# Performance work log

Measured on AMD Instinct MI355X. Metric: run time of the kernel, lower is better.

The kernel has to match this reference:

```python
import jax, jax.numpy as jnp
import numpy as np

B, T, D_MODEL, HEAD_DIM = 8, 2048, 1024, 128


def setup_inputs() -> dict:
    key = jax.random.key(0)
    k1, k2, k3, k4 = jax.random.split(key, 4)
    scale = 1.0 / np.sqrt(D_MODEL)
    return {
        "x": jax.random.normal(k1, (B, T, D_MODEL), dtype=jnp.float32),
        "Wq": jax.random.normal(k2, (HEAD_DIM, D_MODEL), dtype=jnp.float32) * scale,
        "Wk": jax.random.normal(k3, (HEAD_DIM, D_MODEL), dtype=jnp.float32) * scale,
        "Wv": jax.random.normal(k4, (HEAD_DIM, D_MODEL), dtype=jnp.float32) * scale,
    }


def reference(x, Wq, Wk, Wv) -> jnp.ndarray:
    # x: [B, T, C]; torch Linear(no bias): y = x @ W.T, W: [head_dim, d_model]
    q = jnp.einsum("btc,hc->bth", x, Wq)  # [B, T, H]
    k = jnp.einsum("btc,hc->bth", x, Wk)
    v = jnp.einsum("btc,hc->bth", x, Wv)
    head_dim = Wq.shape[0]
    scores = jnp.einsum("bqh,bkh->bqk", q, k) / jnp.sqrt(jnp.float32(head_dim))  # [B, T, T]
    T_ = x.shape[1]
    causal = jnp.tril(jnp.ones((T_, T_), dtype=bool))
    scores = jnp.where(causal, scores, -jnp.inf)
    probs = jax.nn.softmax(scores, axis=-1)
    # dropout is identity at inference (eval mode)
    out = jnp.einsum("bqk,bkh->bqh", probs, v)  # [B, T, head_dim]
    return out
```

## Files before the change

kernel.cpp:

```cpp
#include <hip/hip_runtime.h>
#include <hip/hip_bf16.h>
#include <math.h>

#define T_ 2048
#define C_ 1024
#define H_ 128
#define NB 8
#define WN 131072
#define SC 0.08838834764831845f

typedef __attribute__((ext_vector_type(8))) short bf16x8;
typedef __attribute__((ext_vector_type(8))) unsigned short u16x8;
typedef __attribute__((ext_vector_type(4))) float f32x4;

#define MFMA16(a,b,c) __builtin_amdgcn_mfma_f32_16x16x32_bf16((a),(b),(c),0,0,0)

__device__ __forceinline__ unsigned short f2bf(float f) {
    union { float f; unsigned u; } v; v.f = f;
    unsigned r = v.u + 0x7fffu + ((v.u >> 16) & 1u);
    return (unsigned short)(r >> 16);
}
__device__ __forceinline__ float bf2f(unsigned short u) {
    union { unsigned u; float f; } v; v.u = ((unsigned)u) << 16; return v.f;
}
__device__ __forceinline__ unsigned pk2bf(float a, float b) {
    __hip_bfloat162 h = __float22bfloat162_rn(float2{a, b});
    union { __hip_bfloat162 h; unsigned u; } v; v.h = h; return v.u;
}
__device__ __forceinline__ void gld16(void* lds, const void* g) {
    __builtin_amdgcn_global_load_lds(
        (const __attribute__((address_space(1))) unsigned*)g,
        (__attribute__((address_space(3))) unsigned*)lds, 16, 0, 0);
}

__global__ __launch_bounds__(256) void wconv(const float* __restrict__ Wq,
                                             const float* __restrict__ Wk,
                                             const float* __restrict__ Wv,
                                             unsigned short* __restrict__ Wb) {
    int e = (blockIdx.x * 256 + threadIdx.x) * 8;
    int which = e >> 17;
    int off = e & (WN - 1);
    const float* src = (which == 0) ? Wq : (which == 1 ? Wk : Wv);
    float s = (which == 0) ? SC : 1.0f;
    const float4* p = (const float4*)(src + off);
    float4 a = p[0], b = p[1];
    uint4 o = { pk2bf(a.x * s, a.y * s), pk2bf(a.z * s, a.w * s),
                pk2bf(b.x * s, b.y * s), pk2bf(b.z * s, b.w * s) };
    *(uint4*)(Wb + e) = o;
}

__global__ __launch_bounds__(256, 1) void proj(const float* __restrict__ x,
                                               const unsigned short* __restrict__ Wb,
                                               unsigned short* __restrict__ Q,
                                               unsigned short* __restrict__ K,
                                               unsigned short* __restrict__ V) {
    __shared__ unsigned short Xs[2][2][64][40];
    __shared__ unsigned short Ws[2][2][384][32];

    const int tid  = threadIdx.x;
    const int wave = tid >> 6, lane = tid & 63;
    const int quad = lane >> 4, l16 = lane & 15;
    const int m0   = blockIdx.x * 64;

    f32x4 acc[4][6];
    #pragma unroll
    for (int i = 0; i < 4; i++)
        #pragma unroll
        for (int j = 0; j < 6; j++) acc[i][j] = {0.f, 0.f, 0.f, 0.f};

    const int xrow = tid >> 2, xcg = tid & 3;
    const int xck = xcg >> 1, xco = (xcg & 1) * 16;
    const float* xg = x + (size_t)(m0 + xrow) * C_ + xcg * 16;
    const unsigned short* wg = Wb + (size_t)(wave * 96 + (lane >> 2)) * C_ + (lane & 3) * 8;

    #define STAGE(buf, kc) do {                                                   \
        _Pragma("unroll")                                                         \
        for (int kkc = 0; kkc < 2; kkc++)                                         \
            _Pragma("unroll")                                                     \
            for (int rb = 0; rb < 6; rb++)                                        \
                gld16(&Ws[buf][kkc][wave * 96 + rb * 16][0],                      \
                      wg + (size_t)rb * 16 * C_ + (kc) + kkc * 32);               \
        const float* xp = xg + (kc);                                              \
        float4 f0 = *(const float4*)xp,      f1 = *(const float4*)(xp + 4);       \
        float4 f2 = *(const float4*)(xp + 8), f3 = *(const float4*)(xp + 12);     \
        uint4 u0 = { pk2bf(f0.x,f0.y), pk2bf(f0.z,f0.w),                          \
                     pk2bf(f1.x,f1.y), pk2bf(f1.z,f1.w) };                        \
        uint4 u1 = { pk2bf(f2.x,f2.y), pk2bf(f2.z,f2.w),                          \
                     pk2bf(f3.x,f3.y), pk2bf(f3.z,f3.w) };                        \
        *(uint4*)&Xs[buf][xck][xrow][xco]     = u0;                               \
        *(uint4*)&Xs[buf][xck][xrow][xco + 8] = u1;                               \
    } while (0)

    STAGE(0, 0);
    for (int it = 0; it < 16; it++) {
        __syncthreads();
        if (it < 15) { STAGE((it + 1) & 1, (it + 1) * 64); }
        const int buf = it & 1;
        bf16x8 af[4][2];
        #pragma unroll
        for (int kk = 0; kk < 2; kk++)
            #pragma unroll
            for (int mf = 0; mf < 4; mf++)
                af[mf][kk] = *(bf16x8*)&Xs[buf][kk][mf * 16 + l16][quad * 8];
        #pragma unroll
        for (int kk = 0; kk < 2; kk++)
            #pragma unroll
            for (int nf = 0; nf < 6; nf++) {
                bf16x8 bq = *(bf16x8*)&Ws[buf][kk][wave * 96 + nf * 16 + l16][quad * 8];
                #pragma unroll
                for (int mf = 0; mf < 4; mf++)
                    acc[mf][nf] = MFMA16(af[mf][kk], bq, acc[mf][nf]);
            }
    }
    #undef STAGE

    #pragma unroll
    for (int nf = 0; nf < 6; nf++) {
        int nb = wave * 96 + nf * 16;
        int which = nb >> 7;
        unsigned short* dst = (which == 0) ? Q : (which == 1 ? K : V);
        int c = (nb & 127) + l16;
        #pragma unroll
        for (int mf = 0; mf < 4; mf++)
            #pragma unroll
            for (int r = 0; r < 4; r++)
                dst[(size_t)(m0 + mf * 16 + quad * 4 + r) * H_ + c] = f2bf(acc[mf][nf][r]);
    }
}

__global__ __launch_bounds__(256, 3) void attn(const unsigned short* __restrict__ Qg,
                                               const unsigned short* __restrict__ Kg,
                                               const unsigned short* __restrict__ Vg,
                                               unsigned short* __restrict__ Ob,
                                               float* __restrict__ Ml) {
    const int bx = blockIdx.x;
    const int s  = bx & 7, qt = 31 - (bx >> 3);
    const int b  = blockIdx.y;
    const int qbase = qt * 64, kstart = s * 256;
    if (kstart > qbase) return;
    const int kend  = (kstart + 256 < qbase + 64) ? kstart + 256 : qbase + 64;
    const int niter = (kend - kstart) >> 6;

    __shared__ unsigned short Ks[4][64][32];
    __shared__ unsigned short Vt[128 * 64];
    __shared__ unsigned short Ps[4][16][64];

    const int tid = threadIdx.x, wave = tid >> 6, lane = tid & 63;
    const int quad = lane >> 4, l16 = lane & 15;
    const size_t base = (size_t)b * T_ * H_;

    const unsigned short* ksrc = Kg + base + (size_t)(kstart + (lane >> 2)) * H_ + wave * 32 + (lane & 3) * 8;
    #pragma unroll
    for (int p = 0; p < 4; p++) gld16(&Ks[wave][p * 16][0], ksrc + (size_t)p * 16 * H_);
    const unsigned short* vsrc = Vg + base + (size_t)(kstart + wave * 8 + quad * 2) * H_ + l16 * 8;
    u16x8 vr[2][2];
    vr[0][0] = *(const u16x8*)vsrc;             vr[0][1] = *(const u16x8*)(vsrc + H_);
    vr[1][0] = *(const u16x8*)(vsrc + 32 * H_); vr[1][1] = *(const u16x8*)(vsrc + 33 * H_);

    bf16x8 qf[4];
    const unsigned short* qp = Qg + base + (size_t)(qbase + wave * 16 + l16) * H_ + quad * 8;
    #pragma unroll
    for (int kk = 0; kk < 4; kk++) qf[kk] = *(const bf16x8*)(qp + kk * 32);

    f32x4 o[8];
    #pragma unroll
    for (int i = 0; i < 8; i++) o[i] = {0.f, 0.f, 0.f, 0.f};
    float m_i = -INFINITY, l_i = 0.f;
    const int swz = (l16 & 7) << 3;
    const int qg = qbase + wave * 16 + l16;

    __syncthreads();

    #pragma unroll
    for (int g = 0; g < 2; g++) {
        int t0 = wave * 8 + g * 32 + quad * 2;
        int t8 = t0 >> 3;
        #pragma unroll
        for (int j = 0; j < 8; j++) {
            int h = l16 * 8 + j;
            unsigned pk = (unsigned)(unsigned short)vr[g][0][j] | ((unsigned)(unsigned short)vr[g][1][j] << 16);
            int blk = (t8 ^ (h & 7) ^ ((h >> 3) & 7)) & 7;
            *(unsigned*)&Vt[h * 64 + blk * 8 + (t0 & 7)] = pk;
        }
    }

    for (int kt = 0; ; kt++) {
        const int kbase = kstart + kt * 64;
        f32x4 st[4];
        #pragma unroll
        for (int nf = 0; nf < 4; nf++) st[nf] = {0.f, 0.f, 0.f, 0.f};
        #pragma unroll
        for (int kk = 0; kk < 4; kk++)
            #pragma unroll
            for (int nf = 0; nf < 4; nf++) {
                bf16x8 kfr = *(bf16x8*)&Ks[kk][nf * 16 + l16][quad * 8];
                st[nf] = MFMA16(kfr, qf[kk], st[nf]);
            }
        if (kbase + 64 > qbase) {
            #pragma unroll
            for (int nf = 0; nf < 4; nf++) {
                int kg = kbase + nf * 16 + quad * 4;
                #pragma unroll
                for (int r = 0; r < 4; r++)
                    if (kg + r > qg) st[nf][r] = -INFINITY;
            }
        }
        float mx = st[0][0];
        #pragma unroll
        for (int nf = 0; nf < 4; nf++)
            #pragma unroll
            for (int r = 0; r < 4; r++) mx = fmaxf(mx, st[nf][r]);
        mx = fmaxf(mx, __shfl_xor(mx, 16, 64));
        mx = fmaxf(mx, __shfl_xor(mx, 32, 64));
        float mnew = fmaxf(m_i, mx);
        float al = __expf(m_i - mnew);
        m_i = mnew;
        float rs = 0.f;
        #pragma unroll
        for (int nf = 0; nf < 4; nf++)
            #pragma unroll
            for (int r = 0; r < 4; r++) {
                float e = __expf(st[nf][r] - mnew);
                st[nf][r] = e; rs += e;
            }
        rs += __shfl_xor(rs, 16, 64);
        rs += __shfl_xor(rs, 32, 64);
        l_i = al * l_i + rs;
        #pragma unroll
        for (int nf = 0; nf < 4; nf++) {
            uint2 pk = { pk2bf(st[nf][0], st[nf][1]), pk2bf(st[nf][2], st[nf][3]) };
            *(uint2*)&Ps[wave][l16][(nf * 16 + quad * 4) ^ swz] = pk;
        }
        float a0 = __shfl(al, quad * 4 + 0, 64), a1 = __shfl(al, quad * 4 + 1, 64);
        float a2 = __shfl(al, quad * 4 + 2, 64), a3 = __shfl(al, quad * 4 + 3, 64);
        #pragma unroll
        for (int i = 0; i < 8; i++) {
            o[i][0] *= a0; o[i][1] *= a1; o[i][2] *= a2; o[i][3] *= a3;
        }
        __syncthreads();

        const bool more = (kt + 1 < niter);
        if (more) {
            ksrc += 64 * H_;
            #pragma unroll
            for (int p = 0; p < 4; p++) gld16(&Ks[wave][p * 16][0], ksrc + (size_t)p * 16 * H_);
            vsrc += 64 * H_;
            vr[0][0] = *(const u16x8*)vsrc;             vr[0][1] = *(const u16x8*)(vsrc + H_);
            vr[1][0] = *(const u16x8*)(vsrc + 32 * H_); vr[1][1] = *(const u16x8*)(vsrc + 33 * H_);
        }
        bf16x8 pa0 = *(bf16x8*)&Ps[wave][l16][(quad * 8) ^ swz];
        bf16x8 pa1 = *(bf16x8*)&Ps[wave][l16][(32 + quad * 8) ^ swz];
        #pragma unroll
        for (int nf = 0; nf < 8; nf++) {
            int h = nf * 16 + l16;
            int ex = (h & 7) ^ ((h >> 3) & 7);
            bf16x8 v0 = *(bf16x8*)&Vt[h * 64 + ((quad ^ ex) & 7) * 8];
            bf16x8 v1 = *(bf16x8*)&Vt[h * 64 + (((quad + 4) ^ ex) & 7) * 8];
            o[nf] = MFMA16(pa0, v0, o[nf]);
            o[nf] = MFMA16(pa1, v1, o[nf]);
        }
        if (!more) break;
        __syncthreads();
        #pragma unroll
        for (int g = 0; g < 2; g++) {
            int t0 = wave * 8 + g * 32 + quad * 2;
            int t8 = t0 >> 3;
            #pragma unroll
            for (int j = 0; j < 8; j++) {
                int h = l16 * 8 + j;
                unsigned pk = (unsigned)(unsigned short)vr[g][0][j] | ((unsigned)(unsigned short)vr[g][1][j] << 16);
                int blk = (t8 ^ (h & 7) ^ ((h >> 3) & 7)) & 7;
                *(unsigned*)&Vt[h * 64 + blk * 8 + (t0 & 7)] = pk;
            }
        }
    }

    const int g2 = qt >> 2;
    const int Pq = 2 * g2 * (g2 + 1) + (qt & 3) * (g2 + 1);
    const int slot = (Pq + s) * NB + b;
    float lq[4];
    #pragma unroll
    for (int r = 0; r < 4; r++) lq[r] = __shfl(l_i, quad * 4 + r, 64);
    const size_t obase = (size_t)slot * 64 * 128;
    #pragma unroll
    for (int r = 0; r < 4; r++) {
        float invl = 1.0f / lq[r];
        #pragma unroll
        for (int nf = 0; nf < 8; nf++)
            Ob[obase + (size_t)(wave * 16 + quad * 4 + r) * 128 + nf * 16 + l16] = f2bf(o[nf][r] * invl);
    }
    if (lane < 16) {
        int ridx = slot * 64 + wave * 16 + l16;
        Ml[ridx * 2]     = m_i;
        Ml[ridx * 2 + 1] = l_i;
    }
}

__global__ __launch_bounds__(256) void merge(const unsigned short* __restrict__ Ob,
                                             const float* __restrict__ Ml,
                                             float* __restrict__ out) {
    const int qt = blockIdx.x, b = blockIdx.y;
    const int g = qt >> 2;
    const int Pq = 2 * g * (g + 1) + (qt & 3) * (g + 1);
    const int ns = g + 1;
    const int tid = threadIdx.x;
    const int row = tid >> 2, c0 = (tid & 3) * 32;

    float mv[8], lv[8], mg = -INFINITY;
    for (int s2 = 0; s2 < ns; s2++) {
        int slot = (Pq + s2) * NB + b;
        mv[s2] = Ml[(slot * 64 + row) * 2];
        lv[s2] = Ml[(slot * 64 + row) * 2 + 1];
        mg = fmaxf(mg, mv[s2]);
    }
    float L = 0.f, w[8];
    for (int s2 = 0; s2 < ns; s2++) { w[s2] = lv[s2] * __expf(mv[s2] - mg); L += w[s2]; }
    float inv = 1.0f / L;

    float accv[32];
    #pragma unroll
    for (int i = 0; i < 32; i++) accv[i] = 0.f;
    for (int s2 = 0; s2 < ns; s2++) {
        int slot = (Pq + s2) * NB + b;
        const unsigned short* op = Ob + ((size_t)(slot * 64 + row)) * 128 + c0;
        #pragma unroll
        for (int cc = 0; cc < 4; cc++) {
            u16x8 v = *(const u16x8*)(op + cc * 8);
            #pragma unroll
            for (int j = 0; j < 8; j++) accv[cc * 8 + j] += w[s2] * bf2f(v[j]);
        }
    }
    float* od = out + ((size_t)(b * T_ + qt * 64 + row)) * 128 + c0;
    #pragma unroll
    for (int cc = 0; cc < 8; cc++) {
        float4 w4 = { accv[cc*4] * inv, accv[cc*4+1] * inv, accv[cc*4+2] * inv, accv[cc*4+3] * inv };
        *(float4*)(od + cc * 4) = w4;
    }
}

extern "C" void kernel_launch(void* const* d_in, const int* in_sizes, int n_in,
                              void* d_out, int out_size, void* d_ws, size_t ws_size,
                              hipStream_t stream) {
    const float* x  = (const float*)d_in[0];
    const float* Wq = (const float*)d_in[1];
    const float* Wk = (const float*)d_in[2];
    const float* Wv = (const float*)d_in[3];

    char* ws = (char*)d_ws;
    unsigned short* Wb = (unsigned short*)ws;
    unsigned short* Q  = (unsigned short*)(ws + (size_t) 1 * (1u << 20));
    unsigned short* K  = (unsigned short*)(ws + (size_t) 5 * (1u << 20));
    unsigned short* V  = (unsigned short*)(ws + (size_t) 9 * (1u << 20));
    unsigned short* Ob = (unsigned short*)(ws + (size_t)13 * (1u << 20));
    float*          Ml = (float*)(ws + (size_t)32 * (1u << 20));
    float* out = (float*)d_out;

    hipLaunchKernelGGL(wconv, dim3(192), dim3(256), 0, stream, Wq, Wk, Wv, Wb);
    hipLaunchKernelGGL(proj,  dim3(256), dim3(256), 0, stream, x, Wb, Q, K, V);
    hipLaunchKernelGGL(attn,  dim3(256, NB), dim3(256), 0, stream, Q, K, V, Ob, Ml);
    hipLaunchKernelGGL(merge, dim3(32, NB), dim3(256), 0, stream, Ob, Ml, out);
}
```

Measured before the change: 174.5 us.

## Shrink projection tile to 32 rows and K-step 32 with swizzled W staging

The QKV projection kernel now uses 32-row M tiles and a K step of 32 instead of 64x64, doubling the grid to 512 blocks and raising launch bounds to 2 blocks per CU. Weight tiles staged in LDS get an XOR swizzle on the column chunk to reduce bank conflicts. The aim is to fill all CUs on MI355X (256 blocks underfilled them) and improve latency hiding. In exchange, each weight tile is reused across fewer rows, W traffic from L2 doubles, and there are twice as many sync iterations.

```diff
diff --git a/kernel.cpp b/kernel.cpp
--- a/kernel.cpp
+++ b/kernel.cpp
@@ -49,68 +49,55 @@
     *(uint4*)(Wb + e) = o;
 }
 
-__global__ __launch_bounds__(256, 1) void proj(const float* __restrict__ x,
+__global__ __launch_bounds__(256, 2) void proj(const float* __restrict__ x,
                                                const unsigned short* __restrict__ Wb,
                                                unsigned short* __restrict__ Q,
                                                unsigned short* __restrict__ K,
                                                unsigned short* __restrict__ V) {
-    __shared__ unsigned short Xs[2][2][64][40];
-    __shared__ unsigned short Ws[2][2][384][32];
+    __shared__ unsigned short Xs[2][32][40];
+    __shared__ unsigned short Ws[2][384][32];
 
     const int tid  = threadIdx.x;
     const int wave = tid >> 6, lane = tid & 63;
     const int quad = lane >> 4, l16 = lane & 15;
-    const int m0   = blockIdx.x * 64;
-
-    f32x4 acc[4][6];
-    #pragma unroll
-    for (int i = 0; i < 4; i++)
+    const int m0   = blockIdx.x * 32;
+
+    f32x4 acc[2][6];
+    #pragma unroll
+    for (int i = 0; i < 2; i++)
         #pragma unroll
         for (int j = 0; j < 6; j++) acc[i][j] = {0.f, 0.f, 0.f, 0.f};
 
-    const int xrow = tid >> 2, xcg = tid & 3;
-    const int xck = xcg >> 1, xco = (xcg & 1) * 16;
-    const float* xg = x + (size_t)(m0 + xrow) * C_ + xcg * 16;
-    const unsigned short* wg = Wb + (size_t)(wave * 96 + (lane >> 2)) * C_ + (lane & 3) * 8;
+    const int xrow = tid >> 3, xc4 = (tid & 7) * 4;
+    const float* xg = x + (size_t)(m0 + xrow) * C_ + xc4;
+    const unsigned short* wg = Wb + (size_t)(wave * 96 + (lane >> 2)) * C_
+                               + (size_t)(((lane & 3) ^ ((lane >> 3) & 3)) * 8);
 
     #define STAGE(buf, kc) do {                                                   \
         _Pragma("unroll")                                                         \
-        for (int kkc = 0; kkc < 2; kkc++)                                         \
-            _Pragma("unroll")                                                     \
-            for (int rb = 0; rb < 6; rb++)                                        \
-                gld16(&Ws[buf][kkc][wave * 96 + rb * 16][0],                      \
-                      wg + (size_t)rb * 16 * C_ + (kc) + kkc * 32);               \
-        const float* xp = xg + (kc);                                              \
-        float4 f0 = *(const float4*)xp,      f1 = *(const float4*)(xp + 4);       \
-        float4 f2 = *(const float4*)(xp + 8), f3 = *(const float4*)(xp + 12);     \
-        uint4 u0 = { pk2bf(f0.x,f0.y), pk2bf(f0.z,f0.w),                          \
-                     pk2bf(f1.x,f1.y), pk2bf(f1.z,f1.w) };                        \
-        uint4 u1 = { pk2bf(f2.x,f2.y), pk2bf(f2.z,f2.w),                          \
-                     pk2bf(f3.x,f3.y), pk2bf(f3.z,f3.w) };                        \
-        *(uint4*)&Xs[buf][xck][xrow][xco]     = u0;                               \
-        *(uint4*)&Xs[buf][xck][xrow][xco + 8] = u1;                               \
+        for (int rb = 0; rb < 6; rb++)                                            \
+            gld16(&Ws[buf][wave * 96 + rb * 16][0],                               \
+                  wg + (size_t)rb * 16 * C_ + (kc));                              \
+        float4 f = *(const float4*)(xg + (kc));                                   \
+        *(uint2*)&Xs[buf][xrow][xc4] = uint2{ pk2bf(f.x, f.y), pk2bf(f.z, f.w) }; \
     } while (0)
 
     STAGE(0, 0);
-    for (int it = 0; it < 16; it++) {
+    for (int it = 0; it < 32; it++) {
         __syncthreads();
-        if (it < 15) { STAGE((it + 1) & 1, (it + 1) * 64); }
+        if (it < 31) { STAGE((it + 1) & 1, (it + 1) * 32); }
         const int buf = it & 1;
-        bf16x8 af[4][2];
-        #pragma unroll
-        for (int kk = 0; kk < 2; kk++)
-            #pragma unroll
-            for (int mf = 0; mf < 4; mf++)
-                af[mf][kk] = *(bf16x8*)&Xs[buf][kk][mf * 16 + l16][quad * 8];
-        #pragma unroll
-        for (int kk = 0; kk < 2; kk++)
-            #pragma unroll
-            for (int nf = 0; nf < 6; nf++) {
-                bf16x8 bq = *(bf16x8*)&Ws[buf][kk][wave * 96 + nf * 16 + l16][quad * 8];
-                #pragma unroll
-                for (int mf = 0; mf < 4; mf++)
-                    acc[mf][nf] = MFMA16(af[mf][kk], bq, acc[mf][nf]);
-            }
+        bf16x8 af[2];
+        af[0] = *(bf16x8*)&Xs[buf][l16][quad * 8];
+        af[1] = *(bf16x8*)&Xs[buf][16 + l16][quad * 8];
+        const int rsw = (l16 >> 1) & 3;
+        #pragma unroll
+        for (int nf = 0; nf < 6; nf++) {
+            int row = wave * 96 + nf * 16 + l16;
+            bf16x8 bq = *(bf16x8*)&Ws[buf][row][(quad ^ rsw) * 8];
+            acc[0][nf] = MFMA16(af[0], bq, acc[0][nf]);
+            acc[1][nf] = MFMA16(af[1], bq, acc[1][nf]);
+        }
     }
     #undef STAGE
 
@@ -121,7 +108,7 @@
         unsigned short* dst = (which == 0) ? Q : (which == 1 ? K : V);
         int c = (nb & 127) + l16;
         #pragma unroll
-        for (int mf = 0; mf < 4; mf++)
+        for (int mf = 0; mf < 2; mf++)
             #pragma unroll
             for (int r = 0; r < 4; r++)
                 dst[(size_t)(m0 + mf * 16 + quad * 4 + r) * H_ + c] = f2bf(acc[mf][nf][r]);
@@ -356,7 +343,7 @@
     float* out = (float*)d_out;
 
     hipLaunchKernelGGL(wconv, dim3(192), dim3(256), 0, stream, Wq, Wk, Wv, Wb);
-    hipLaunchKernelGGL(proj,  dim3(256), dim3(256), 0, stream, x, Wb, Q, K, V);
+    hipLaunchKernelGGL(proj,  dim3(512), dim3(256), 0, stream, x, Wb, Q, K, V);
     hipLaunchKernelGGL(attn,  dim3(256, NB), dim3(256), 0, stream, Q, K, V, Ob, Ml);
     hipLaunchKernelGGL(merge, dim3(32, NB), dim3(256), 0, stream, Ob, Ml, out);
 }
```

New measurement: 181.7 us. 4.1% more time.
